# Kernel optimization log

Measured on AMD Instinct MI355X. Metric: run time of the kernel, lower is better.

Reference implementation:

```python
import jax, jax.numpy as jnp
import numpy as np

SEQ_LEN = 1024
DIM = 384
QK_DIM = 64
BATCH = 16


def setup_inputs() -> dict:
    key = jax.random.key(0)
    k_x, k_qw, k_qb, k_kw = jax.random.split(key, 4)
    bound = DIM ** (-0.5)
    x = jax.random.normal(k_x, (BATCH, SEQ_LEN, DIM), dtype=jnp.float32)
    # ColumnLinear params: weight [seq_len, out_features, in_features]
    q_weight = jax.random.uniform(k_qw, (SEQ_LEN, QK_DIM, DIM), minval=-bound, maxval=bound, dtype=jnp.float32)
    q_bias = jnp.zeros((SEQ_LEN, QK_DIM), dtype=jnp.float32)  # init zeros; keep as param
    k_weight = jax.random.uniform(k_kw, (SEQ_LEN, QK_DIM, DIM), minval=-bound, maxval=bound, dtype=jnp.float32)
    attn_bias = jnp.zeros((SEQ_LEN, SEQ_LEN), dtype=jnp.float32)
    return {"x": x, "q_weight": q_weight, "q_bias": q_bias, "k_weight": k_weight, "attn_bias": attn_bias}


def reference(x, q_weight, q_bias, k_weight, attn_bias):
    scale = DIM ** (-0.5)  # note: scale uses dim, not qk_dim
    # per-column (untied) linear projections
    q = scale * (jnp.einsum('bnc,ndc->bnd', x, q_weight) + q_bias)  # [B,S,qk]
    k = jnp.einsum('bnc,ndc->bnd', x, k_weight)                     # [B,S,qk]
    attn = jnp.einsum('bnd,bmd->bnm', q, k) + attn_bias             # [B,S,S]
    attn = jax.nn.softmax(attn, axis=-1)
    out = jnp.einsum('bnm,bmc->bnc', attn, x)                       # value = input
    return out, attn
```

## Files before the change

kernel.cpp:

```cpp
#include <hip/hip_runtime.h>

#define B_  16
#define S_  1024
#define D_  384
#define QK_ 64

typedef __attribute__((ext_vector_type(8))) short bf16x8;
typedef __attribute__((ext_vector_type(4))) short bf16x4;
typedef __attribute__((ext_vector_type(4))) float f32x4;

__device__ __forceinline__ short f2bf(float f) {
  union { float f; unsigned u; } v; v.f = f;
  unsigned r = v.u + 0x7FFFu + ((v.u >> 16) & 1u);
  return (short)(r >> 16);
}

__device__ __forceinline__ bf16x4 cvt4(const float4 v) {
  bf16x4 r;
  r[0] = f2bf(v.x); r[1] = f2bf(v.y); r[2] = f2bf(v.z); r[3] = f2bf(v.w);
  return r;
}

__global__ __launch_bounds__(256) void k_proj(
    const float* __restrict__ x, const float* __restrict__ qw,
    const float* __restrict__ qb, const float* __restrict__ kw,
    unsigned short* __restrict__ Qb, unsigned short* __restrict__ Kb) {
  __shared__ __attribute__((aligned(16))) short xs[16 * 392];

  const int pos  = blockIdx.x >> 1;
  const int half = blockIdx.x & 1;
  const int tid  = threadIdx.x;
  const int lane = tid & 63;
  const int w    = tid >> 6;
  const int col  = lane & 15;
  const int quad = lane >> 4;

  float4 xv[6];
#pragma unroll
  for (int r = 0; r < 6; ++r) {
    int li = tid + 256 * r;
    int brow = li / 96, c4 = li % 96;
    xv[r] = *(const float4*)&x[(brow * S_ + pos) * D_ + 4 * c4];
  }

  const float* wsrc = half ? kw : qw;
  const int j = w * 16 + col;
  const float* wrow = &wsrc[((size_t)pos * QK_ + j) * D_];

  float4 wv[8];
#pragma unroll
  for (int ks = 0; ks < 4; ++ks) {
    wv[2 * ks]     = *(const float4*)&wrow[ks * 32 + quad * 8];
    wv[2 * ks + 1] = *(const float4*)&wrow[ks * 32 + quad * 8 + 4];
  }

#pragma unroll
  for (int r = 0; r < 6; ++r) {
    int li = tid + 256 * r;
    int brow = li / 96, c4 = li % 96;
    *(bf16x4*)&xs[brow * 392 + 4 * c4] = cvt4(xv[r]);
  }
  __syncthreads();

  f32x4 acc = {0.f, 0.f, 0.f, 0.f};
#pragma unroll
  for (int ks = 0; ks < 12; ++ks) {
    const int sl = ks & 3;
    bf16x8 aF = *(const bf16x8*)&xs[col * 392 + ks * 32 + quad * 8];
    bf16x4 lo = cvt4(wv[2 * sl]), hi = cvt4(wv[2 * sl + 1]);
    if (ks < 8) {
      wv[2 * sl]     = *(const float4*)&wrow[(ks + 4) * 32 + quad * 8];
      wv[2 * sl + 1] = *(const float4*)&wrow[(ks + 4) * 32 + quad * 8 + 4];
    }
    bf16x8 bF;
    bF[0] = lo[0]; bF[1] = lo[1]; bF[2] = lo[2]; bF[3] = lo[3];
    bF[4] = hi[0]; bF[5] = hi[1]; bF[6] = hi[2]; bF[7] = hi[3];
    acc = __builtin_amdgcn_mfma_f32_16x16x32_bf16(aF, bF, acc, 0, 0, 0);
  }

  const float SCALE = 0.051031036307982884f;
#pragma unroll
  for (int r = 0; r < 4; ++r) {
    const int brow = quad * 4 + r;
    float v = acc[r];
    if (half == 0) {
      v = SCALE * (v + qb[pos * QK_ + j]);
      Qb[(brow * S_ + pos) * QK_ + j] = (unsigned short)f2bf(v);
    } else {
      Kb[(brow * S_ + pos) * QK_ + j] = (unsigned short)f2bf(v);
    }
  }
}

__global__ __launch_bounds__(256) void k_xt(
    const float* __restrict__ x, unsigned short* __restrict__ Xt) {
  __shared__ float T[32][33];
  const int gid = blockIdx.x;
  const int b  = gid / (32 * 12);
  const int r  = gid % (32 * 12);
  const int jt = r / 12, ct = r % 12;
  const int j0 = jt * 32, c0 = ct * 32;
  const int tx = threadIdx.x & 31, ty = threadIdx.x >> 5;
#pragma unroll
  for (int k = 0; k < 4; ++k)
    T[ty + 8 * k][tx] = x[(size_t)(b * S_ + j0 + ty + 8 * k) * D_ + c0 + tx];
  __syncthreads();
#pragma unroll
  for (int k = 0; k < 4; ++k) {
    int c = ty + 8 * k;
    Xt[((size_t)b * D_ + c0 + c) * S_ + j0 + tx] = (unsigned short)f2bf(T[tx][c]);
  }
}

__global__ __launch_bounds__(64) void k_attn(
    const unsigned short* __restrict__ Qb, const unsigned short* __restrict__ Kb,
    const float* __restrict__ bias, float* __restrict__ attn) {
  const int gid   = blockIdx.x;
  const int b     = gid >> 6;
  const int i0    = (gid & 63) * 16;
  const int lane  = threadIdx.x & 63;
  const int col   = lane & 15, quad = lane >> 4;
  const int iq    = i0 + quad * 4;

  const unsigned short* qp = &Qb[(size_t)(b * S_ + i0 + col) * QK_];
  const bf16x8 qf0 = *(const bf16x8*)&qp[quad * 8];
  const bf16x8 qf1 = *(const bf16x8*)&qp[32 + quad * 8];

  float m[4] = {-3.0e38f, -3.0e38f, -3.0e38f, -3.0e38f};
  float l[4] = {0.f, 0.f, 0.f, 0.f};

  for (int jt = 0; jt < 16; ++jt) {
    const int j0 = jt * 64;
    const unsigned short* kp = &Kb[(size_t)(b * S_ + j0 + col) * QK_];
    f32x4 acc[4] = {{0.f,0.f,0.f,0.f},{0.f,0.f,0.f,0.f},
                    {0.f,0.f,0.f,0.f},{0.f,0.f,0.f,0.f}};
#pragma unroll
    for (int s = 0; s < 4; ++s) {
      bf16x8 k0 = *(const bf16x8*)&kp[(s * 16) * QK_ + quad * 8];
      bf16x8 k1 = *(const bf16x8*)&kp[(s * 16) * QK_ + 32 + quad * 8];
      acc[s] = __builtin_amdgcn_mfma_f32_16x16x32_bf16(qf0, k0, acc[s], 0, 0, 0);
      acc[s] = __builtin_amdgcn_mfma_f32_16x16x32_bf16(qf1, k1, acc[s], 0, 0, 0);
    }
#pragma unroll
    for (int r = 0; r < 4; ++r) {
      float sv0 = acc[0][r] + bias[(size_t)(iq + r) * S_ + j0 + 0 * 16 + col];
      float sv1 = acc[1][r] + bias[(size_t)(iq + r) * S_ + j0 + 1 * 16 + col];
      float sv2 = acc[2][r] + bias[(size_t)(iq + r) * S_ + j0 + 2 * 16 + col];
      float sv3 = acc[3][r] + bias[(size_t)(iq + r) * S_ + j0 + 3 * 16 + col];
      float t = fmaxf(fmaxf(sv0, sv1), fmaxf(sv2, sv3));
#pragma unroll
      for (int off = 8; off >= 1; off >>= 1) t = fmaxf(t, __shfl_xor(t, off));
      const float mn = fmaxf(m[r], t);
      float sum = __expf(sv0 - mn) + __expf(sv1 - mn) +
                  __expf(sv2 - mn) + __expf(sv3 - mn);
#pragma unroll
      for (int off = 8; off >= 1; off >>= 1) sum += __shfl_xor(sum, off);
      l[r] = l[r] * __expf(m[r] - mn) + sum;
      m[r] = mn;
    }
  }

  float inv[4];
#pragma unroll
  for (int r = 0; r < 4; ++r) inv[r] = 1.0f / l[r];

  for (int jt = 0; jt < 16; ++jt) {
    const int j0 = jt * 64;
    const unsigned short* kp = &Kb[(size_t)(b * S_ + j0 + col) * QK_];
    f32x4 acc[4] = {{0.f,0.f,0.f,0.f},{0.f,0.f,0.f,0.f},
                    {0.f,0.f,0.f,0.f},{0.f,0.f,0.f,0.f}};
#pragma unroll
    for (int s = 0; s < 4; ++s) {
      bf16x8 k0 = *(const bf16x8*)&kp[(s * 16) * QK_ + quad * 8];
      bf16x8 k1 = *(const bf16x8*)&kp[(s * 16) * QK_ + 32 + quad * 8];
      acc[s] = __builtin_amdgcn_mfma_f32_16x16x32_bf16(qf0, k0, acc[s], 0, 0, 0);
      acc[s] = __builtin_amdgcn_mfma_f32_16x16x32_bf16(qf1, k1, acc[s], 0, 0, 0);
    }
#pragma unroll
    for (int r = 0; r < 4; ++r) {
#pragma unroll
      for (int s = 0; s < 4; ++s) {
        const float sv = acc[s][r] +
            bias[(size_t)(iq + r) * S_ + j0 + s * 16 + col];
        attn[(size_t)(b * S_ + iq + r) * S_ + j0 + s * 16 + col] =
            __expf(sv - m[r]) * inv[r];
      }
    }
  }
}

__global__ __launch_bounds__(256) void k_out(
    const float* __restrict__ attn, const unsigned short* __restrict__ Xt,
    float* __restrict__ out) {
  __shared__ __attribute__((aligned(16))) short Ps[64 * 72];
  __shared__ __attribute__((aligned(16))) short Xs[128 * 72];
  const int gid0 = blockIdx.x;
  const int gid  = (gid0 & 7) * 96 + (gid0 >> 3);
  const int b = gid / 48, r48 = gid % 48;
  const int it = r48 / 3, ct = r48 % 3;
  const int i0 = it * 64, c0 = ct * 128;
  const int tid = threadIdx.x, lane = tid & 63, w = tid >> 6;
  const int col = lane & 15, quad = lane >> 4;

  const float* pA = &attn[(size_t)(b * S_ + i0) * S_];
  const unsigned short* xA = &Xt[((size_t)b * D_ + c0) * S_];

  f32x4 acc[8] = {{0.f,0.f,0.f,0.f},{0.f,0.f,0.f,0.f},{0.f,0.f,0.f,0.f},
                  {0.f,0.f,0.f,0.f},{0.f,0.f,0.f,0.f},{0.f,0.f,0.f,0.f},
                  {0.f,0.f,0.f,0.f},{0.f,0.f,0.f,0.f}};

  float4 pv[4];
  uint4  xv[4];

#pragma unroll
  for (int r = 0; r < 4; ++r) {
    int li = tid + 256 * r;
    { int ii = li >> 4, f4 = li & 15;
      pv[r] = *(const float4*)&pA[(size_t)ii * S_ + f4 * 4]; }
    { int cc = li >> 3, p8 = li & 7;
      xv[r] = *(const uint4*)&xA[(size_t)cc * S_ + p8 * 8]; }
  }

  for (int t = 0; t < 16; ++t) {
    __syncthreads();
#pragma unroll
    for (int r = 0; r < 4; ++r) {
      int li = tid + 256 * r;
      int ii = li >> 4, f4 = li & 15;
      *(bf16x4*)&Ps[ii * 72 + f4 * 4] = cvt4(pv[r]);
    }
#pragma unroll
    for (int r = 0; r < 4; ++r) {
      int li = tid + 256 * r;
      int cc = li >> 3, p8 = li & 7;
      *(uint4*)&Xs[cc * 72 + p8 * 8] = xv[r];
    }
    __syncthreads();
    if (t < 15) {
      const int j1 = (t + 1) * 64;
#pragma unroll
      for (int r = 0; r < 4; ++r) {
        int li = tid + 256 * r;
        { int ii = li >> 4, f4 = li & 15;
          pv[r] = *(const float4*)&pA[(size_t)ii * S_ + j1 + f4 * 4]; }
        { int cc = li >> 3, p8 = li & 7;
          xv[r] = *(const uint4*)&xA[(size_t)cc * S_ + j1 + p8 * 8]; }
      }
    }
#pragma unroll
    for (int ks = 0; ks < 2; ++ks) {
      bf16x8 aF = *(const bf16x8*)&Ps[(w * 16 + col) * 72 + ks * 32 + quad * 8];
#pragma unroll
      for (int s = 0; s < 8; ++s) {
        bf16x8 bF = *(const bf16x8*)&Xs[(s * 16 + col) * 72 + ks * 32 + quad * 8];
        acc[s] = __builtin_amdgcn_mfma_f32_16x16x32_bf16(aF, bF, acc[s], 0, 0, 0);
      }
    }
  }

#pragma unroll
  for (int s = 0; s < 8; ++s) {
    const int c = c0 + s * 16 + col;
#pragma unroll
    for (int r = 0; r < 4; ++r) {
      const int i = i0 + w * 16 + quad * 4 + r;
      out[(size_t)(b * S_ + i) * D_ + c] = acc[s][r];
    }
  }
}

extern "C" void kernel_launch(void* const* d_in, const int* in_sizes, int n_in,
                              void* d_out, int out_size, void* d_ws, size_t ws_size,
                              hipStream_t stream) {
  const float* x  = (const float*)d_in[0];
  const float* qw = (const float*)d_in[1];
  const float* qb = (const float*)d_in[2];
  const float* kw = (const float*)d_in[3];
  const float* ab = (const float*)d_in[4];

  float* out  = (float*)d_out;
  float* attn = out + (size_t)B_ * S_ * D_;

  unsigned short* Qb = (unsigned short*)d_ws;
  unsigned short* Kb = Qb + (size_t)B_ * S_ * QK_;
  unsigned short* Xt = Kb + (size_t)B_ * S_ * QK_;

  k_proj <<<2 * S_,       256, 0, stream>>>(x, qw, qb, kw, Qb, Kb);
  k_xt   <<<B_ * 32 * 12, 256, 0, stream>>>(x, Xt);
  k_attn <<<B_ * 64,       64, 0, stream>>>(Qb, Kb, ab, attn);
  k_out  <<<B_ * 16 * 3,  256, 0, stream>>>(attn, Xt, out);
}
```

Baseline: 381.1 us.

## Split attention key range across four waves and prefetch all projection weights

k_attn now runs four waves per 16-row block. Each wave handles a quarter of the key range and computes a partial max and sum, and the partials are merged through shared memory before the normalized probabilities are written. This gives four times the wave parallelism for the softmax/attn-write kernel, which previously used only one wave per block and 1024 blocks. k_proj also fully unrolls and issues all 12 weight loads up front instead of keeping a 4-deep rotating prefetch. That raises register pressure in exchange for more memory-level parallelism.

Measured after the change: 364.4 us. 1.05x faster.

```diff
diff --git a/kernel.cpp b/kernel.cpp
--- a/kernel.cpp
+++ b/kernel.cpp
@@ -35,48 +35,43 @@
   const int col  = lane & 15;
   const int quad = lane >> 4;
 
-  float4 xv[6];
-#pragma unroll
-  for (int r = 0; r < 6; ++r) {
-    int li = tid + 256 * r;
-    int brow = li / 96, c4 = li % 96;
-    xv[r] = *(const float4*)&x[(brow * S_ + pos) * D_ + 4 * c4];
-  }
+  float4 xv0, xv1, xv2, xv3, xv4, xv5;
+#define XL(r, dst) { const int li = tid + 256 * (r);                        \
+    const int brow = li / 96, c4 = li % 96;                                 \
+    dst = *(const float4*)&x[(brow * S_ + pos) * D_ + 4 * c4]; }
+  XL(0, xv0) XL(1, xv1) XL(2, xv2) XL(3, xv3) XL(4, xv4) XL(5, xv5)
+#undef XL
 
   const float* wsrc = half ? kw : qw;
   const int j = w * 16 + col;
   const float* wrow = &wsrc[((size_t)pos * QK_ + j) * D_];
 
-  float4 wv[8];
-#pragma unroll
-  for (int ks = 0; ks < 4; ++ks) {
-    wv[2 * ks]     = *(const float4*)&wrow[ks * 32 + quad * 8];
-    wv[2 * ks + 1] = *(const float4*)&wrow[ks * 32 + quad * 8 + 4];
-  }
-
-#pragma unroll
-  for (int r = 0; r < 6; ++r) {
-    int li = tid + 256 * r;
-    int brow = li / 96, c4 = li % 96;
-    *(bf16x4*)&xs[brow * 392 + 4 * c4] = cvt4(xv[r]);
-  }
+  float4 wA0, wB0, wA1, wB1, wA2,  wB2,  wA3,  wB3,  wA4,  wB4,  wA5,  wB5,
+         wA6, wB6, wA7, wB7, wA8,  wB8,  wA9,  wB9,  wA10, wB10, wA11, wB11;
+#define WL(k)                                                               \
+  wA##k = *(const float4*)&wrow[(k) * 32 + quad * 8];                       \
+  wB##k = *(const float4*)&wrow[(k) * 32 + quad * 8 + 4];
+  WL(0) WL(1) WL(2) WL(3) WL(4) WL(5) WL(6) WL(7) WL(8) WL(9) WL(10) WL(11)
+#undef WL
+
+#define XS(r, src) { const int li = tid + 256 * (r);                        \
+    const int brow = li / 96, c4 = li % 96;                                 \
+    *(bf16x4*)&xs[brow * 392 + 4 * c4] = cvt4(src); }
+  XS(0, xv0) XS(1, xv1) XS(2, xv2) XS(3, xv3) XS(4, xv4) XS(5, xv5)
+#undef XS
   __syncthreads();
 
   f32x4 acc = {0.f, 0.f, 0.f, 0.f};
-#pragma unroll
-  for (int ks = 0; ks < 12; ++ks) {
-    const int sl = ks & 3;
-    bf16x8 aF = *(const bf16x8*)&xs[col * 392 + ks * 32 + quad * 8];
-    bf16x4 lo = cvt4(wv[2 * sl]), hi = cvt4(wv[2 * sl + 1]);
-    if (ks < 8) {
-      wv[2 * sl]     = *(const float4*)&wrow[(ks + 4) * 32 + quad * 8];
-      wv[2 * sl + 1] = *(const float4*)&wrow[(ks + 4) * 32 + quad * 8 + 4];
-    }
-    bf16x8 bF;
-    bF[0] = lo[0]; bF[1] = lo[1]; bF[2] = lo[2]; bF[3] = lo[3];
-    bF[4] = hi[0]; bF[5] = hi[1]; bF[6] = hi[2]; bF[7] = hi[3];
-    acc = __builtin_amdgcn_mfma_f32_16x16x32_bf16(aF, bF, acc, 0, 0, 0);
-  }
+#define STEP(k) {                                                           \
+    bf16x8 aF = *(const bf16x8*)&xs[col * 392 + (k) * 32 + quad * 8];       \
+    bf16x4 lo = cvt4(wA##k), hi = cvt4(wB##k);                              \
+    bf16x8 bF;                                                              \
+    bF[0] = lo[0]; bF[1] = lo[1]; bF[2] = lo[2]; bF[3] = lo[3];             \
+    bF[4] = hi[0]; bF[5] = hi[1]; bF[6] = hi[2]; bF[7] = hi[3];             \
+    acc = __builtin_amdgcn_mfma_f32_16x16x32_bf16(aF, bF, acc, 0, 0, 0); }
+  STEP(0) STEP(1) STEP(2) STEP(3) STEP(4)  STEP(5)
+  STEP(6) STEP(7) STEP(8) STEP(9) STEP(10) STEP(11)
+#undef STEP
 
   const float SCALE = 0.051031036307982884f;
 #pragma unroll
@@ -112,13 +107,15 @@
   }
 }
 
-__global__ __launch_bounds__(64) void k_attn(
+__global__ __launch_bounds__(256) void k_attn(
     const unsigned short* __restrict__ Qb, const unsigned short* __restrict__ Kb,
     const float* __restrict__ bias, float* __restrict__ attn) {
+  __shared__ float Ms[4][16], Ls[4][16];
   const int gid   = blockIdx.x;
   const int b     = gid >> 6;
   const int i0    = (gid & 63) * 16;
-  const int lane  = threadIdx.x & 63;
+  const int tid   = threadIdx.x;
+  const int lane  = tid & 63, w = tid >> 6;
   const int col   = lane & 15, quad = lane >> 4;
   const int iq    = i0 + quad * 4;
 
@@ -129,8 +126,9 @@
   float m[4] = {-3.0e38f, -3.0e38f, -3.0e38f, -3.0e38f};
   float l[4] = {0.f, 0.f, 0.f, 0.f};
 
-  for (int jt = 0; jt < 16; ++jt) {
-    const int j0 = jt * 64;
+#pragma unroll
+  for (int jj = 0; jj < 4; ++jj) {
+    const int j0 = (w * 4 + jj) * 64;
     const unsigned short* kp = &Kb[(size_t)(b * S_ + j0 + col) * QK_];
     f32x4 acc[4] = {{0.f,0.f,0.f,0.f},{0.f,0.f,0.f,0.f},
                     {0.f,0.f,0.f,0.f},{0.f,0.f,0.f,0.f}};
@@ -160,12 +158,31 @@
     }
   }
 
-  float inv[4];
-#pragma unroll
-  for (int r = 0; r < 4; ++r) inv[r] = 1.0f / l[r];
-
-  for (int jt = 0; jt < 16; ++jt) {
-    const int j0 = jt * 64;
+  if (col == 0) {
+#pragma unroll
+    for (int r = 0; r < 4; ++r) {
+      Ms[w][quad * 4 + r] = m[r];
+      Ls[w][quad * 4 + r] = l[r];
+    }
+  }
+  __syncthreads();
+
+  float gm[4], inv[4];
+#pragma unroll
+  for (int r = 0; r < 4; ++r) {
+    const int row = quad * 4 + r;
+    const float m0 = Ms[0][row], m1 = Ms[1][row];
+    const float m2 = Ms[2][row], m3 = Ms[3][row];
+    const float g  = fmaxf(fmaxf(m0, m1), fmaxf(m2, m3));
+    const float L  = Ls[0][row] * __expf(m0 - g) + Ls[1][row] * __expf(m1 - g)
+                   + Ls[2][row] * __expf(m2 - g) + Ls[3][row] * __expf(m3 - g);
+    gm[r]  = g;
+    inv[r] = 1.0f / L;
+  }
+
+#pragma unroll
+  for (int jj = 0; jj < 4; ++jj) {
+    const int j0 = (w * 4 + jj) * 64;
     const unsigned short* kp = &Kb[(size_t)(b * S_ + j0 + col) * QK_];
     f32x4 acc[4] = {{0.f,0.f,0.f,0.f},{0.f,0.f,0.f,0.f},
                     {0.f,0.f,0.f,0.f},{0.f,0.f,0.f,0.f}};
@@ -183,7 +200,7 @@
         const float sv = acc[s][r] +
             bias[(size_t)(iq + r) * S_ + j0 + s * 16 + col];
         attn[(size_t)(b * S_ + iq + r) * S_ + j0 + s * 16 + col] =
-            __expf(sv - m[r]) * inv[r];
+            __expf(sv - gm[r]) * inv[r];
       }
     }
   }
@@ -287,6 +304,6 @@
 
   k_proj <<<2 * S_,       256, 0, stream>>>(x, qw, qb, kw, Qb, Kb);
   k_xt   <<<B_ * 32 * 12, 256, 0, stream>>>(x, Xt);
-  k_attn <<<B_ * 64,       64, 0, stream>>>(Qb, Kb, ab, attn);
+  k_attn <<<B_ * 64,      256, 0, stream>>>(Qb, Kb, ab, attn);
   k_out  <<<B_ * 16 * 3,  256, 0, stream>>>(attn, Xt, out);
 }
```

## Fuse softmax and attn@V into one kernel, stage projection weights in LDS

Applied to the files above, without the earlier changes.

Merges the attention-softmax and output-matmul kernels into a single kernel. Each 256-thread block handles 32 query rows, with two waves per 16-row strip splitting the key range for the max/sum pass and merging their partial statistics through shared memory. The second pass writes the attention probabilities to global memory and also stores them as bf16 in LDS, then multiplies them directly by the transposed x read from global memory. This avoids re-reading the large fp32 attention matrix. Separately, the projection kernel loads its whole weight tile with coalesced nontemporal loads into a swizzled LDS buffer instead of per-lane strided loads. Risks include only 512 blocks for the fused kernel, B fragments fetched uncached from global memory, extra barriers per tile, and higher LDS use in the projection kernel lowering occupancy.

New measurement: 375.7 us. No clear change (-1.4%).

```diff
diff --git a/kernel.cpp b/kernel.cpp
--- a/kernel.cpp
+++ b/kernel.cpp
@@ -18,6 +18,12 @@
 __device__ __forceinline__ bf16x4 cvt4(const float4 v) {
   bf16x4 r;
   r[0] = f2bf(v.x); r[1] = f2bf(v.y); r[2] = f2bf(v.z); r[3] = f2bf(v.w);
+  return r;
+}
+
+__device__ __forceinline__ bf16x4 cvt4v(const f32x4 v) {
+  bf16x4 r;
+  r[0] = f2bf(v[0]); r[1] = f2bf(v[1]); r[2] = f2bf(v[2]); r[3] = f2bf(v[3]);
   return r;
 }
 
@@ -26,6 +32,7 @@
     const float* __restrict__ qb, const float* __restrict__ kw,
     unsigned short* __restrict__ Qb, unsigned short* __restrict__ Kb) {
   __shared__ __attribute__((aligned(16))) short xs[16 * 392];
+  __shared__ __attribute__((aligned(16))) short ws[64 * 384];
 
   const int pos  = blockIdx.x >> 1;
   const int half = blockIdx.x & 1;
@@ -43,15 +50,14 @@
     xv[r] = *(const float4*)&x[(brow * S_ + pos) * D_ + 4 * c4];
   }
 
-  const float* wsrc = half ? kw : qw;
-  const int j = w * 16 + col;
-  const float* wrow = &wsrc[((size_t)pos * QK_ + j) * D_];
-
-  float4 wv[8];
-#pragma unroll
-  for (int ks = 0; ks < 4; ++ks) {
-    wv[2 * ks]     = *(const float4*)&wrow[ks * 32 + quad * 8];
-    wv[2 * ks + 1] = *(const float4*)&wrow[ks * 32 + quad * 8 + 4];
+  const float* wsrc  = half ? kw : qw;
+  const float* wbase = wsrc + (size_t)pos * 64 * D_;
+
+  f32x4 wv[24];
+#pragma unroll
+  for (int r = 0; r < 24; ++r) {
+    const int li = tid + 256 * r;
+    wv[r] = __builtin_nontemporal_load((const f32x4*)(wbase + 4 * (size_t)li));
   }
 
 #pragma unroll
@@ -60,21 +66,22 @@
     int brow = li / 96, c4 = li % 96;
     *(bf16x4*)&xs[brow * 392 + 4 * c4] = cvt4(xv[r]);
   }
+#pragma unroll
+  for (int r = 0; r < 24; ++r) {
+    const int li  = tid + 256 * r;
+    const int row = li / 96, c4 = li % 96;
+    const int idx = (row * 384 + 4 * c4) ^ ((row & 7) << 3);
+    *(bf16x4*)&ws[idx] = cvt4v(wv[r]);
+  }
   __syncthreads();
 
+  const int jrow = w * 16 + col;
+  const int xor3 = (jrow & 7) << 3;
   f32x4 acc = {0.f, 0.f, 0.f, 0.f};
 #pragma unroll
   for (int ks = 0; ks < 12; ++ks) {
-    const int sl = ks & 3;
     bf16x8 aF = *(const bf16x8*)&xs[col * 392 + ks * 32 + quad * 8];
-    bf16x4 lo = cvt4(wv[2 * sl]), hi = cvt4(wv[2 * sl + 1]);
-    if (ks < 8) {
-      wv[2 * sl]     = *(const float4*)&wrow[(ks + 4) * 32 + quad * 8];
-      wv[2 * sl + 1] = *(const float4*)&wrow[(ks + 4) * 32 + quad * 8 + 4];
-    }
-    bf16x8 bF;
-    bF[0] = lo[0]; bF[1] = lo[1]; bF[2] = lo[2]; bF[3] = lo[3];
-    bF[4] = hi[0]; bF[5] = hi[1]; bF[6] = hi[2]; bF[7] = hi[3];
+    bf16x8 bF = *(const bf16x8*)&ws[(jrow * 384 + ks * 32 + quad * 8) ^ xor3];
     acc = __builtin_amdgcn_mfma_f32_16x16x32_bf16(aF, bF, acc, 0, 0, 0);
   }
 
@@ -84,10 +91,10 @@
     const int brow = quad * 4 + r;
     float v = acc[r];
     if (half == 0) {
-      v = SCALE * (v + qb[pos * QK_ + j]);
-      Qb[(brow * S_ + pos) * QK_ + j] = (unsigned short)f2bf(v);
+      v = SCALE * (v + qb[pos * QK_ + jrow]);
+      Qb[(brow * S_ + pos) * QK_ + jrow] = (unsigned short)f2bf(v);
     } else {
-      Kb[(brow * S_ + pos) * QK_ + j] = (unsigned short)f2bf(v);
+      Kb[(brow * S_ + pos) * QK_ + jrow] = (unsigned short)f2bf(v);
     }
   }
 }
@@ -112,25 +119,33 @@
   }
 }
 
-__global__ __launch_bounds__(64) void k_attn(
+__global__ __launch_bounds__(256) void k_fused(
     const unsigned short* __restrict__ Qb, const unsigned short* __restrict__ Kb,
-    const float* __restrict__ bias, float* __restrict__ attn) {
-  const int gid   = blockIdx.x;
-  const int b     = gid >> 6;
-  const int i0    = (gid & 63) * 16;
-  const int lane  = threadIdx.x & 63;
-  const int col   = lane & 15, quad = lane >> 4;
-  const int iq    = i0 + quad * 4;
-
-  const unsigned short* qp = &Qb[(size_t)(b * S_ + i0 + col) * QK_];
+    const float* __restrict__ bias, const unsigned short* __restrict__ Xt,
+    float* __restrict__ attn, float* __restrict__ out) {
+  __shared__ float Ms[2][2][16], Ls[2][2][16];
+  __shared__ __attribute__((aligned(16))) short Ps[32 * 72];
+
+  const int gid0 = blockIdx.x;
+  const int gid  = (gid0 & 7) * 64 + (gid0 >> 3);
+  const int b  = gid >> 5;
+  const int i0 = (gid & 31) * 32;
+  const int tid = threadIdx.x, lane = tid & 63, w = tid >> 6;
+  const int is = w >> 1, h = w & 1;
+  const int col = lane & 15, quad = lane >> 4;
+  const int ib = i0 + is * 16;
+  const int iq = ib + quad * 4;
+
+  const unsigned short* qp = &Qb[(size_t)(b * S_ + ib + col) * QK_];
   const bf16x8 qf0 = *(const bf16x8*)&qp[quad * 8];
   const bf16x8 qf1 = *(const bf16x8*)&qp[32 + quad * 8];
 
   float m[4] = {-3.0e38f, -3.0e38f, -3.0e38f, -3.0e38f};
   float l[4] = {0.f, 0.f, 0.f, 0.f};
 
-  for (int jt = 0; jt < 16; ++jt) {
-    const int j0 = jt * 64;
+#pragma unroll
+  for (int st = 0; st < 8; ++st) {
+    const int j0 = (h * 8 + st) * 64;
     const unsigned short* kp = &Kb[(size_t)(b * S_ + j0 + col) * QK_];
     f32x4 acc[4] = {{0.f,0.f,0.f,0.f},{0.f,0.f,0.f,0.f},
                     {0.f,0.f,0.f,0.f},{0.f,0.f,0.f,0.f}};
@@ -160,111 +175,77 @@
     }
   }
 
-  float inv[4];
-#pragma unroll
-  for (int r = 0; r < 4; ++r) inv[r] = 1.0f / l[r];
+  if (col == 0) {
+#pragma unroll
+    for (int r = 0; r < 4; ++r) {
+      Ms[is][h][quad * 4 + r] = m[r];
+      Ls[is][h][quad * 4 + r] = l[r];
+    }
+  }
+  __syncthreads();
+
+  float gm[4], inv[4];
+#pragma unroll
+  for (int r = 0; r < 4; ++r) {
+    const int row = quad * 4 + r;
+    const float m0 = Ms[is][0][row], m1 = Ms[is][1][row];
+    const float g  = fmaxf(m0, m1);
+    const float L  = Ls[is][0][row] * __expf(m0 - g) +
+                     Ls[is][1][row] * __expf(m1 - g);
+    gm[r]  = g;
+    inv[r] = 1.0f / L;
+  }
+
+  f32x4 oacc[12] = {{0.f,0.f,0.f,0.f},{0.f,0.f,0.f,0.f},{0.f,0.f,0.f,0.f},
+                    {0.f,0.f,0.f,0.f},{0.f,0.f,0.f,0.f},{0.f,0.f,0.f,0.f},
+                    {0.f,0.f,0.f,0.f},{0.f,0.f,0.f,0.f},{0.f,0.f,0.f,0.f},
+                    {0.f,0.f,0.f,0.f},{0.f,0.f,0.f,0.f},{0.f,0.f,0.f,0.f}};
+  const unsigned short* xb = &Xt[((size_t)b * D_ + h * 192) * S_];
 
   for (int jt = 0; jt < 16; ++jt) {
     const int j0 = jt * 64;
     const unsigned short* kp = &Kb[(size_t)(b * S_ + j0 + col) * QK_];
-    f32x4 acc[4] = {{0.f,0.f,0.f,0.f},{0.f,0.f,0.f,0.f},
-                    {0.f,0.f,0.f,0.f},{0.f,0.f,0.f,0.f}};
-#pragma unroll
-    for (int s = 0; s < 4; ++s) {
+    f32x4 a2[2] = {{0.f,0.f,0.f,0.f},{0.f,0.f,0.f,0.f}};
+#pragma unroll
+    for (int ss = 0; ss < 2; ++ss) {
+      const int s = 2 * h + ss;
       bf16x8 k0 = *(const bf16x8*)&kp[(s * 16) * QK_ + quad * 8];
       bf16x8 k1 = *(const bf16x8*)&kp[(s * 16) * QK_ + 32 + quad * 8];
-      acc[s] = __builtin_amdgcn_mfma_f32_16x16x32_bf16(qf0, k0, acc[s], 0, 0, 0);
-      acc[s] = __builtin_amdgcn_mfma_f32_16x16x32_bf16(qf1, k1, acc[s], 0, 0, 0);
-    }
+      a2[ss] = __builtin_amdgcn_mfma_f32_16x16x32_bf16(qf0, k0, a2[ss], 0, 0, 0);
+      a2[ss] = __builtin_amdgcn_mfma_f32_16x16x32_bf16(qf1, k1, a2[ss], 0, 0, 0);
+    }
+    __syncthreads();
+#pragma unroll
+    for (int ss = 0; ss < 2; ++ss) {
+      const int s = 2 * h + ss;
+#pragma unroll
+      for (int r = 0; r < 4; ++r) {
+        const float sv = a2[ss][r] +
+            bias[(size_t)(iq + r) * S_ + j0 + s * 16 + col];
+        const float p = __expf(sv - gm[r]) * inv[r];
+        attn[(size_t)(b * S_ + iq + r) * S_ + j0 + s * 16 + col] = p;
+        Ps[(is * 16 + quad * 4 + r) * 72 + s * 16 + col] = f2bf(p);
+      }
+    }
+    __syncthreads();
+#pragma unroll
+    for (int ks = 0; ks < 2; ++ks) {
+      bf16x8 aF = *(const bf16x8*)&Ps[(is * 16 + col) * 72 + ks * 32 + quad * 8];
+#pragma unroll
+      for (int cs = 0; cs < 12; ++cs) {
+        bf16x8 bF = *(const bf16x8*)
+            &xb[(size_t)(cs * 16 + col) * S_ + j0 + ks * 32 + quad * 8];
+        oacc[cs] = __builtin_amdgcn_mfma_f32_16x16x32_bf16(aF, bF, oacc[cs], 0, 0, 0);
+      }
+    }
+  }
+
+#pragma unroll
+  for (int cs = 0; cs < 12; ++cs) {
+    const int c = h * 192 + cs * 16 + col;
 #pragma unroll
     for (int r = 0; r < 4; ++r) {
-#pragma unroll
-      for (int s = 0; s < 4; ++s) {
-        const float sv = acc[s][r] +
-            bias[(size_t)(iq + r) * S_ + j0 + s * 16 + col];
-        attn[(size_t)(b * S_ + iq + r) * S_ + j0 + s * 16 + col] =
-            __expf(sv - m[r]) * inv[r];
-      }
-    }
-  }
-}
-
-__global__ __launch_bounds__(256) void k_out(
-    const float* __restrict__ attn, const unsigned short* __restrict__ Xt,
-    float* __restrict__ out) {
-  __shared__ __attribute__((aligned(16))) short Ps[64 * 72];
-  __shared__ __attribute__((aligned(16))) short Xs[128 * 72];
-  const int gid0 = blockIdx.x;
-  const int gid  = (gid0 & 7) * 96 + (gid0 >> 3);
-  const int b = gid / 48, r48 = gid % 48;
-  const int it = r48 / 3, ct = r48 % 3;
-  const int i0 = it * 64, c0 = ct * 128;
-  const int tid = threadIdx.x, lane = tid & 63, w = tid >> 6;
-  const int col = lane & 15, quad = lane >> 4;
-
-  const float* pA = &attn[(size_t)(b * S_ + i0) * S_];
-  const unsigned short* xA = &Xt[((size_t)b * D_ + c0) * S_];
-
-  f32x4 acc[8] = {{0.f,0.f,0.f,0.f},{0.f,0.f,0.f,0.f},{0.f,0.f,0.f,0.f},
-                  {0.f,0.f,0.f,0.f},{0.f,0.f,0.f,0.f},{0.f,0.f,0.f,0.f},
-                  {0.f,0.f,0.f,0.f},{0.f,0.f,0.f,0.f}};
-
-  float4 pv[4];
-  uint4  xv[4];
-
-#pragma unroll
-  for (int r = 0; r < 4; ++r) {
-    int li = tid + 256 * r;
-    { int ii = li >> 4, f4 = li & 15;
-      pv[r] = *(const float4*)&pA[(size_t)ii * S_ + f4 * 4]; }
-    { int cc = li >> 3, p8 = li & 7;
-      xv[r] = *(const uint4*)&xA[(size_t)cc * S_ + p8 * 8]; }
-  }
-
-  for (int t = 0; t < 16; ++t) {
-    __syncthreads();
-#pragma unroll
-    for (int r = 0; r < 4; ++r) {
-      int li = tid + 256 * r;
-      int ii = li >> 4, f4 = li & 15;
-      *(bf16x4*)&Ps[ii * 72 + f4 * 4] = cvt4(pv[r]);
-    }
-#pragma unroll
-    for (int r = 0; r < 4; ++r) {
-      int li = tid + 256 * r;
-      int cc = li >> 3, p8 = li & 7;
-      *(uint4*)&Xs[cc * 72 + p8 * 8] = xv[r];
-    }
-    __syncthreads();
-    if (t < 15) {
-      const int j1 = (t + 1) * 64;
-#pragma unroll
-      for (int r = 0; r < 4; ++r) {
-        int li = tid + 256 * r;
-        { int ii = li >> 4, f4 = li & 15;
-          pv[r] = *(const float4*)&pA[(size_t)ii * S_ + j1 + f4 * 4]; }
-        { int cc = li >> 3, p8 = li & 7;
-          xv[r] = *(const uint4*)&xA[(size_t)cc * S_ + j1 + p8 * 8]; }
-      }
-    }
-#pragma unroll
-    for (int ks = 0; ks < 2; ++ks) {
-      bf16x8 aF = *(const bf16x8*)&Ps[(w * 16 + col) * 72 + ks * 32 + quad * 8];
-#pragma unroll
-      for (int s = 0; s < 8; ++s) {
-        bf16x8 bF = *(const bf16x8*)&Xs[(s * 16 + col) * 72 + ks * 32 + quad * 8];
-        acc[s] = __builtin_amdgcn_mfma_f32_16x16x32_bf16(aF, bF, acc[s], 0, 0, 0);
-      }
-    }
-  }
-
-#pragma unroll
-  for (int s = 0; s < 8; ++s) {
-    const int c = c0 + s * 16 + col;
-#pragma unroll
-    for (int r = 0; r < 4; ++r) {
-      const int i = i0 + w * 16 + quad * 4 + r;
-      out[(size_t)(b * S_ + i) * D_ + c] = acc[s][r];
+      out[(size_t)(b * S_ + iq + r) * D_ + c] = oacc[cs][r];
     }
   }
 }
@@ -285,8 +266,7 @@
   unsigned short* Kb = Qb + (size_t)B_ * S_ * QK_;
   unsigned short* Xt = Kb + (size_t)B_ * S_ * QK_;
 
-  k_proj <<<2 * S_,       256, 0, stream>>>(x, qw, qb, kw, Qb, Kb);
-  k_xt   <<<B_ * 32 * 12, 256, 0, stream>>>(x, Xt);
-  k_attn <<<B_ * 64,       64, 0, stream>>>(Qb, Kb, ab, attn);
-  k_out  <<<B_ * 16 * 3,  256, 0, stream>>>(attn, Xt, out);
-}
+  k_proj  <<<2 * S_,       256, 0, stream>>>(x, qw, qb, kw, Qb, Kb);
+  k_xt    <<<B_ * 32 * 12, 256, 0, stream>>>(x, Xt);
+  k_fused <<<B_ * 32,      256, 0, stream>>>(Qb, Kb, ab, Xt, attn, out);
+}
```
